# Kernel optimization log

Hardware: AMD Instinct MI355X
Metric: run time of the kernel (lower is better)

Reference implementation:

```python
import jax, jax.numpy as jnp
import numpy as np

B, T, H, S, NH = 8, 4096, 1024, 64, 16
DH = H // NH
L = T // S  # tokens per sentence (contiguous partition)


def setup_inputs() -> dict:
    key = jax.random.key(0)
    ks = jax.random.split(key, 10)
    init = lambda k, shape: (jax.random.normal(k, shape, dtype=jnp.float32) * 0.02)
    starts = jnp.arange(S, dtype=jnp.int32) * L
    bounds = jnp.stack([starts, starts + L], axis=-1)  # [S,2]
    sentence_boundaries = jnp.broadcast_to(bounds, (B, S, 2))
    return {
        "context_hidden": jax.random.normal(ks[0], (B, T, H), dtype=jnp.float32),
        "sentence_boundaries": sentence_boundaries,
        "in_proj_w": init(ks[1], (3 * H, H)),
        "in_proj_b": jnp.zeros((3 * H,), jnp.float32),
        "out_w": init(ks[2], (H, H)),
        "out_b": jnp.zeros((H,), jnp.float32),
        "w1": init(ks[3], (H, 2 * H)),
        "b1": jnp.zeros((H,), jnp.float32),
        "w2": init(ks[4], (1, H)),
        "b2": jnp.zeros((1,), jnp.float32),
    }


def _forward(h, sentence_boundaries, in_proj_w, in_proj_b, out_w, out_b, w1, b1, w2, b2):
    starts = sentence_boundaries[:, :, 0]  # [B,S]
    ends = sentence_boundaries[:, :, 1]    # [B,S]
    t = jnp.arange(T, dtype=jnp.int32)
    # membership: token t belongs to sentence s iff start <= t < end
    member = (t[None, :, None] >= starts[:, None, :]) & (t[None, :, None] < ends[:, None, :])  # [B,T,S]
    mf = member.astype(h.dtype)
    counts = jnp.clip(mf.sum(axis=1), 1.0)  # [B,S]
    # segment mean pooling (encode_sentences)
    sent_repr = jnp.einsum('bts,bth->bsh', mf, h) / counts[..., None]  # [B,S,H]

    # multihead self-attention over sentence reprs (eval mode, no dropout)
    qkv = sent_repr @ in_proj_w.T + in_proj_b  # [B,S,3H]
    q, k, v = jnp.split(qkv, 3, axis=-1)
    q = q.reshape(B, S, NH, DH)
    k = k.reshape(B, S, NH, DH)
    v = v.reshape(B, S, NH, DH)
    scores = jnp.einsum('bqhd,bkhd->bhqk', q, k) / jnp.sqrt(jnp.asarray(DH, h.dtype))
    attn = jax.nn.softmax(scores, axis=-1)
    ctx = jnp.einsum('bhqk,bkhd->bqhd', attn, v).reshape(B, S, H)
    attended = ctx @ out_w.T + out_b  # [B,S,H]

    # gather each token's sentence repr
    sid = jnp.clip(member.astype(jnp.int32).argmax(axis=-1), 0, S - 1)  # [B,T]
    covered = member.any(axis=-1)  # [B,T]
    att_tok = jnp.take_along_axis(attended, sid[..., None], axis=1)  # [B,T,H]

    # coherence scorer MLP on concat([token, sent_repr]) without materializing concat
    hid = jax.nn.relu(h @ w1[:, :H].T + att_tok @ w1[:, H:].T + b1)  # [B,T,H]
    score = (hid @ w2.T + b2)[..., 0]  # [B,T]
    score = jnp.where(covered, score, 0.0)
    return h + score[..., None] * h


def reference(context_hidden, sentence_boundaries, in_proj_w, in_proj_b, out_w, out_b, w1, b1, w2, b2):
    return _forward(context_hidden, sentence_boundaries, in_proj_w, in_proj_b,
                    out_w, out_b, w1, b1, w2, b2)
```

## Files before the change

kernel.cpp:

```cpp
#include <hip/hip_runtime.h>
#include <stdint.h>

#define BB 8
#define TT 4096
#define HH 1024
#define SS 64
#define NHH 16
#define DHH 64

typedef __attribute__((ext_vector_type(8))) short short8;
typedef __attribute__((ext_vector_type(8))) unsigned short ushortx8;
typedef __attribute__((ext_vector_type(4))) float f32x4;
typedef unsigned short u16;

#define GLOAD16(gp, lp)                                                   \
  __builtin_amdgcn_global_load_lds(                                      \
      (const __attribute__((address_space(1))) void*)(gp),               \
      (__attribute__((address_space(3))) void*)(lp), 16, 0, 0)

__device__ __forceinline__ u16 f2bf(float f) {
  union { float f; uint32_t u; } v;
  v.f = f;
  uint32_t u = v.u;
  uint32_t r = u + 0x7fffu + ((u >> 16) & 1u);
  return (u16)(r >> 16);
}

__device__ __forceinline__ float bf2f(u16 b) {
  union { uint32_t u; float f; } v;
  v.u = ((uint32_t)b) << 16;
  return v.f;
}

__device__ __forceinline__ void stage_tile(u16* lds, const float* src, int ld, int tid) {
#pragma unroll
  for (int q = 0; q < 4; ++q) {
    int slot_id = tid + (q << 8);
    int row = slot_id >> 3;
    int sl = slot_id & 7;
    const float* p = src + (size_t)row * ld + (sl << 3);
    float4 x0 = *(const float4*)(p);
    float4 x1 = *(const float4*)(p + 4);
    ushortx8 o;
    o[0] = f2bf(x0.x); o[1] = f2bf(x0.y); o[2] = f2bf(x0.z); o[3] = f2bf(x0.w);
    o[4] = f2bf(x1.x); o[5] = f2bf(x1.y); o[6] = f2bf(x1.z); o[7] = f2bf(x1.w);
    *(ushortx8*)(&lds[(row << 6) + (((sl ^ (row & 7)) << 3))]) = o;
  }
}

__global__ __launch_bounds__(256) void conv_setup_kernel(const float* __restrict__ h,
                                                         u16* __restrict__ hbf,
                                                         const float* __restrict__ w1,
                                                         u16* __restrict__ wbf,
                                                         const float* __restrict__ ipb,
                                                         const float* __restrict__ outb,
                                                         const float* __restrict__ b1,
                                                         const int* __restrict__ bounds,
                                                         float* __restrict__ qkv,
                                                         float* __restrict__ att,
                                                         float* __restrict__ cbuf,
                                                         int* __restrict__ sid) {
  int bid = blockIdx.x;
  int tid = threadIdx.x;
  if (bid >= 4224) {
    int sidx = (bid - 4224) * 256 + tid;
    const int STR = 512 * 256;
    for (int i = sidx; i < 512 * 3072; i += STR) qkv[i] = ipb[i % 3072];
    for (int i = sidx; i < 512 * 1024; i += STR) att[i] = outb[i & 1023];
    for (int i = sidx; i < 512 * 1024; i += STR) cbuf[i] = b1[i & 1023];
    if (sidx < BB * TT) {
      int b = sidx >> 12, t = sidx & (TT - 1);
      int r = -1;
      for (int s = 0; s < SS; ++s) {
        int st = bounds[(b * SS + s) * 2], en = bounds[(b * SS + s) * 2 + 1];
        if (t >= st && t < en) { r = s; break; }
      }
      sid[sidx] = r;
    }
    return;
  }
  const float* src;
  int ld, tbid;
  u16* dst;
  if (bid < 4096) { src = h;  ld = 1024; dst = hbf; tbid = bid; }
  else            { src = w1; ld = 2048; dst = wbf; tbid = bid - 4096; }
  int rt = tbid >> 4, kt = tbid & 15;
  const float* s0 = src + (size_t)rt * 128 * ld + kt * 64;
  u16* d0 = dst + (size_t)tbid * 8192;
#pragma unroll
  for (int q = 0; q < 4; ++q) {
    int slot_id = tid + (q << 8);
    int row = slot_id >> 3;
    int sl = slot_id & 7;
    const float* p = s0 + (size_t)row * ld + (sl << 3);
    float4 x0 = *(const float4*)(p);
    float4 x1 = *(const float4*)(p + 4);
    ushortx8 o;
    o[0] = f2bf(x0.x); o[1] = f2bf(x0.y); o[2] = f2bf(x0.z); o[3] = f2bf(x0.w);
    o[4] = f2bf(x1.x); o[5] = f2bf(x1.y); o[6] = f2bf(x1.z); o[7] = f2bf(x1.w);
    *(ushortx8*)(&d0[(row << 6) + (((sl ^ (row & 7)) << 3))]) = o;
  }
}

__global__ __launch_bounds__(256) void pool_bf_kernel(const u16* __restrict__ hbf,
                                                      const int* __restrict__ bounds,
                                                      float* __restrict__ sent) {
  int bs = blockIdx.x;
  int b = bs >> 6;
  int start = bounds[bs * 2];
  int end = bounds[bs * 2 + 1];
  int lo = max(start, 0), hi = min(end, TT);
  int cnt = max(hi - lo, 0);
  float inv = 1.0f / (float)max(cnt, 1);
  int tid = threadIdx.x;
  int sg = tid >> 1;
  int half = tid & 1;
  int kt = sg >> 3, slot = sg & 7;
  float a[8] = {};
  for (int t = lo + half; t < hi; t += 2) {
    int grow = b * TT + t;
    int rt = grow >> 7, r = grow & 127;
    const u16* tile = hbf + ((size_t)rt * 16 + kt) * 8192;
    ushortx8 v = *(const ushortx8*)(&tile[(r << 6) + ((slot ^ (r & 7)) << 3)]);
#pragma unroll
    for (int j = 0; j < 8; ++j) a[j] += bf2f(v[j]);
  }
#pragma unroll
  for (int j = 0; j < 8; ++j) a[j] += __shfl_xor(a[j], 1);
  if (half == 0) {
    float* d = sent + (size_t)bs * HH + sg * 8;
#pragma unroll
    for (int j = 0; j < 8; ++j) d[j] = a[j] * inv;
  }
}

__global__ __launch_bounds__(256) void gemm_bt_atomic(const float* __restrict__ A, int lda,
                                                      const float* __restrict__ Bm, int ldb,
                                                      float* __restrict__ C, int ldc,
                                                      int kper) {
  __shared__ u16 As[128 * 64];
  __shared__ u16 Bs[128 * 64];
  int tid = threadIdx.x;
  int m0 = blockIdx.x * 128, n0 = blockIdx.y * 128;
  int kbeg = blockIdx.z * kper;
  f32x4 acc[4][4] = {};

  for (int k0 = kbeg; k0 < kbeg + kper; k0 += 64) {
    __syncthreads();
    stage_tile(As, A + (size_t)m0 * lda + k0, lda, tid);
    stage_tile(Bs, Bm + (size_t)n0 * ldb + k0, ldb, tid);
    __syncthreads();
    int lane = tid & 63, wid = tid >> 6;
    int wm = wid >> 1, wn = wid & 1;
    int lr = lane & 15, lg = lane >> 4;
#pragma unroll
    for (int kk = 0; kk < 2; ++kk) {
      short8 af[4], bfr[4];
#pragma unroll
      for (int i = 0; i < 4; ++i) {
        int arow = wm * 64 + i * 16 + lr;
        int aslot = (kk * 4 + lg) ^ (arow & 7);
        af[i] = *(const short8*)(&As[(arow << 6) + (aslot << 3)]);
        int brow = wn * 64 + i * 16 + lr;
        int bslot = (kk * 4 + lg) ^ (brow & 7);
        bfr[i] = *(const short8*)(&Bs[(brow << 6) + (bslot << 3)]);
      }
#pragma unroll
      for (int i = 0; i < 4; ++i)
#pragma unroll
        for (int j = 0; j < 4; ++j)
          acc[i][j] = __builtin_amdgcn_mfma_f32_16x16x32_bf16(af[i], bfr[j], acc[i][j], 0, 0, 0);
    }
  }

  int lane = tid & 63, wid = tid >> 6;
  int wm = wid >> 1, wn = wid & 1;
  int lr = lane & 15, lg = lane >> 4;
#pragma unroll
  for (int i = 0; i < 4; ++i)
#pragma unroll
    for (int j = 0; j < 4; ++j)
#pragma unroll
      for (int r = 0; r < 4; ++r) {
        int row = m0 + wm * 64 + i * 16 + lg * 4 + r;
        int col = n0 + wn * 64 + j * 16 + lr;
        atomicAdd(&C[(size_t)row * ldc + col], acc[i][j][r]);
      }
}

__global__ __launch_bounds__(256) void attn_kernel(const float* __restrict__ qkv,
                                                   float* __restrict__ ctx) {
  int bh = blockIdx.x;
  int b = bh >> 4, nh = bh & 15;
  __shared__ float q[64][64], k[64][64], v[64][64], s[64][64];
  int tid = threadIdx.x;
  const float* base = qkv + (size_t)b * SS * 3072 + nh * 64;
  for (int e = tid; e < 4096; e += 256) {
    int i = e >> 6, d = e & 63;
    q[i][d] = base[(size_t)i * 3072 + d];
    k[i][d] = base[(size_t)i * 3072 + 1024 + d];
    v[i][d] = base[(size_t)i * 3072 + 2048 + d];
  }
  __syncthreads();
  for (int e = tid; e < 4096; e += 256) {
    int i = e >> 6, j = e & 63;
    float acc = 0.f;
#pragma unroll 8
    for (int d = 0; d < 64; ++d) acc += q[i][d] * k[j][d];
    s[i][j] = acc * 0.125f;
  }
  __syncthreads();
  {
    int r = tid >> 2, sub = tid & 3;
    int j0 = sub * 16;
    float m = -1e30f;
#pragma unroll
    for (int j = 0; j < 16; ++j) m = fmaxf(m, s[r][j0 + j]);
    m = fmaxf(m, __shfl_xor(m, 1));
    m = fmaxf(m, __shfl_xor(m, 2));
    float sum = 0.f;
#pragma unroll
    for (int j = 0; j < 16; ++j) {
      float e_ = __expf(s[r][j0 + j] - m);
      s[r][j0 + j] = e_;
      sum += e_;
    }
    sum += __shfl_xor(sum, 1);
    sum += __shfl_xor(sum, 2);
    float inv = 1.0f / sum;
#pragma unroll
    for (int j = 0; j < 16; ++j) s[r][j0 + j] *= inv;
  }
  __syncthreads();
  for (int e = tid; e < 4096; e += 256) {
    int i = e >> 6, d = e & 63;
    float acc = 0.f;
#pragma unroll 8
    for (int j = 0; j < 64; ++j) acc += s[i][j] * v[j][d];
    ctx[((size_t)b * SS + i) * HH + nh * 64 + d] = acc;
  }
}

__global__ __launch_bounds__(512, 4) void score_partial(const u16* __restrict__ hbf,
                                                        const u16* __restrict__ wbf,
                                                        const float* __restrict__ cbuf,
                                                        const float* __restrict__ w2,
                                                        const int* __restrict__ sid_arr,
                                                        float* __restrict__ score_part) {
  __shared__ u16 As[8192];
  __shared__ u16 Bs[16384];
  __shared__ float w2_lds[256];
  __shared__ int sid_lds[128];
  __shared__ float red[128];

  int tid = threadIdx.x;
  int bid = blockIdx.x;
  int x = bid & 7;
  int g = bid >> 3;
  int mt = x * 32 + (g >> 2);
  int c = g & 3;
  int n0 = c * 256;
  size_t g0 = (size_t)mt * 128;
  int b = (int)(g0 >> 12);
  const u16* asrc = hbf + (size_t)mt * 16 * 8192;

  if (tid < 256) w2_lds[tid] = w2[n0 + tid];
  if (tid < 128) {
    sid_lds[tid] = sid_arr[g0 + tid];
    red[tid] = 0.f;
  }

  int lane = tid & 63, wid = tid >> 6;
  int wm = wid >> 2, wn = wid & 3;
  int lr = lane & 15, lg = lane >> 4;

  f32x4 acc[4][4] = {};
  for (int kt = 0; kt < 16; ++kt) {
    __syncthreads();
    const u16* at = asrc + kt * 8192;
#pragma unroll
    for (int q = 0; q < 2; ++q) {
      int off = q * 4096 + wid * 512;
      GLOAD16(at + off + lane * 8, &As[off]);
    }
#pragma unroll
    for (int q = 0; q < 4; ++q) {
      int half = q >> 1;
      int boff = (q & 1) * 4096 + wid * 512;
      const u16* bt = wbf + ((size_t)(2 * c + half) * 16 + kt) * 8192;
      GLOAD16(bt + boff + lane * 8, &Bs[half * 8192 + boff]);
    }
    __syncthreads();
#pragma unroll
    for (int kk = 0; kk < 2; ++kk) {
      short8 af[4], bfr[4];
#pragma unroll
      for (int i = 0; i < 4; ++i) {
        int arow = wm * 64 + i * 16 + lr;
        int aslot = (kk * 4 + lg) ^ (arow & 7);
        af[i] = *(const short8*)(&As[(arow << 6) + (aslot << 3)]);
      }
#pragma unroll
      for (int j = 0; j < 4; ++j) {
        int brow = wn * 64 + j * 16 + lr;
        int half = (wn * 64 + j * 16) >> 7;
        int r = brow & 127;
        int bslot = (kk * 4 + lg) ^ (r & 7);
        bfr[j] = *(const short8*)(&Bs[(half << 13) + (r << 6) + (bslot << 3)]);
      }
#pragma unroll
      for (int i = 0; i < 4; ++i)
#pragma unroll
        for (int j = 0; j < 4; ++j)
          acc[i][j] = __builtin_amdgcn_mfma_f32_16x16x32_bf16(af[i], bfr[j], acc[i][j], 0, 0, 0);
    }
  }

  float sp[4][4];
#pragma unroll
  for (int i = 0; i < 4; ++i) {
#pragma unroll
    for (int r = 0; r < 4; ++r) {
      int rowl = wm * 64 + i * 16 + lg * 4 + r;
      int s = sid_lds[rowl];
      int sc = s < 0 ? 0 : s;
      const float* crow = cbuf + ((size_t)b * SS + sc) * HH + n0;
      float accs = 0.f;
#pragma unroll
      for (int j = 0; j < 4; ++j) {
        int coll = wn * 64 + j * 16 + lr;
        float t = acc[i][j][r] + crow[coll];
        if (t > 0.f) accs += t * w2_lds[coll];
      }
      sp[i][r] = accs;
    }
  }

#pragma unroll
  for (int i = 0; i < 4; ++i)
#pragma unroll
    for (int r = 0; r < 4; ++r) {
      float v = sp[i][r];
      v += __shfl_xor(v, 1);
      v += __shfl_xor(v, 2);
      v += __shfl_xor(v, 4);
      v += __shfl_xor(v, 8);
      sp[i][r] = v;
    }
  if (lr == 0) {
#pragma unroll
    for (int i = 0; i < 4; ++i)
#pragma unroll
      for (int r = 0; r < 4; ++r)
        atomicAdd(&red[wm * 64 + i * 16 + lg * 4 + r], sp[i][r]);
  }
  __syncthreads();
  if (tid < 128) score_part[(size_t)c * (BB * TT) + g0 + tid] = red[tid];
}

__global__ __launch_bounds__(256) void scale_kernel(const u16* __restrict__ hbf,
                                                    const float* __restrict__ score_part,
                                                    const float* __restrict__ b2,
                                                    const int* __restrict__ sid_arr,
                                                    float* __restrict__ out) {
  __shared__ float fac[16];
  int tid = threadIdx.x;
  int r0 = blockIdx.x * 16;
  if (tid < 16) {
    int t = r0 + tid;
    float s = b2[0];
#pragma unroll
    for (int c = 0; c < 4; ++c) s += score_part[(size_t)c * (BB * TT) + t];
    fac[tid] = (sid_arr[t] >= 0) ? (1.0f + s) : 1.0f;
  }
  __syncthreads();
  for (int e = tid; e < 16 * 128; e += 256) {
    int row = e >> 7, grp = e & 127;
    int kt = grp >> 3, slot = grp & 7;
    int grow = r0 + row;
    int rt = grow >> 7, r = grow & 127;
    const u16* tile = hbf + ((size_t)rt * 16 + kt) * 8192;
    ushortx8 v = *(const ushortx8*)(&tile[(r << 6) + ((slot ^ (r & 7)) << 3)]);
    float f = fac[row];
    float4 o0, o1;
    o0.x = bf2f(v[0]) * f; o0.y = bf2f(v[1]) * f; o0.z = bf2f(v[2]) * f; o0.w = bf2f(v[3]) * f;
    o1.x = bf2f(v[4]) * f; o1.y = bf2f(v[5]) * f; o1.z = bf2f(v[6]) * f; o1.w = bf2f(v[7]) * f;
    float4* dst = (float4*)(out + (size_t)grow * HH + grp * 8);
    dst[0] = o0;
    dst[1] = o1;
  }
}

extern "C" void kernel_launch(void* const* d_in, const int* in_sizes, int n_in,
                              void* d_out, int out_size, void* d_ws, size_t ws_size,
                              hipStream_t stream) {
  const float* h        = (const float*)d_in[0];
  const int*   bounds   = (const int*)d_in[1];
  const float* in_proj_w = (const float*)d_in[2];
  const float* in_proj_b = (const float*)d_in[3];
  const float* out_w    = (const float*)d_in[4];
  const float* out_b    = (const float*)d_in[5];
  const float* w1       = (const float*)d_in[6];
  const float* b1       = (const float*)d_in[7];
  const float* w2       = (const float*)d_in[8];
  const float* b2       = (const float*)d_in[9];
  float* out = (float*)d_out;

  char* ws = (char*)d_ws;
  float* sent  = (float*)(ws);
  float* qkv   = (float*)(ws + (2ull << 20));
  float* ctx   = (float*)(ws + (8ull << 20));
  float* att   = (float*)(ws + (10ull << 20));
  float* cbuf  = (float*)(ws + (12ull << 20));
  int*   sid   = (int*)(ws + (14ull << 20));
  float* spart = (float*)(ws + (15ull << 20));
  u16*   hbf   = (u16*)(ws + (16ull << 20));
  u16*   wbf   = (u16*)(ws + (80ull << 20));

  conv_setup_kernel<<<4096 + 128 + 512, 256, 0, stream>>>(
      h, hbf, w1, wbf, in_proj_b, out_b, b1, bounds, qkv, att, cbuf, sid);

  pool_bf_kernel<<<BB * SS, 256, 0, stream>>>(hbf, bounds, sent);

  gemm_bt_atomic<<<dim3(4, 24, 4), 256, 0, stream>>>(sent, HH, in_proj_w, HH, qkv, 3 * HH, 256);
  attn_kernel<<<BB * NHH, 256, 0, stream>>>(qkv, ctx);
  gemm_bt_atomic<<<dim3(4, 8, 4), 256, 0, stream>>>(ctx, HH, out_w, HH, att, HH, 256);
  gemm_bt_atomic<<<dim3(4, 8, 4), 256, 0, stream>>>(att, HH, w1 + HH, 2 * HH, cbuf, HH, 256);

  score_partial<<<1024, 512, 0, stream>>>(hbf, wbf, cbuf, w2, sid, spart);
  scale_kernel<<<2048, 256, 0, stream>>>(hbf, spart, b2, sid, out);
}
```

Measured before the change: 282.5 us.

## Fuse sentence pooling, attention and projection GEMMs into one cooperative kernel

Replaces five small back-to-back launches (pooling, QKV GEMM, attention, out-proj GEMM, w1 GEMM) with a single cooperative kernel of 512 blocks that uses grid-wide syncs between phases. The aim is to remove per-launch overhead and inter-kernel gaps on a chain of tiny kernels. In exchange it adds grid.sync costs, requires all 512 blocks co-resident (the 64KB LDS allocation limits occupancy), and leaves many blocks idle in the later phases.

```diff
diff --git a/kernel.cpp b/kernel.cpp
--- a/kernel.cpp
+++ b/kernel.cpp
@@ -1,5 +1,8 @@
 #include <hip/hip_runtime.h>
+#include <hip/hip_cooperative_groups.h>
 #include <stdint.h>
+
+namespace cg = cooperative_groups;
 
 #define BB 8
 #define TT 4096
@@ -46,6 +49,51 @@
     o[4] = f2bf(x1.x); o[5] = f2bf(x1.y); o[6] = f2bf(x1.z); o[7] = f2bf(x1.w);
     *(ushortx8*)(&lds[(row << 6) + (((sl ^ (row & 7)) << 3))]) = o;
   }
+}
+
+__device__ __forceinline__ void gemm_tile_body(const float* A, int lda,
+                                               const float* Bm, int ldb,
+                                               float* C, int ldc,
+                                               int m0, int n0, int kbeg, int kend,
+                                               u16* As, u16* Bs, int tid) {
+  f32x4 acc[4][4] = {};
+  int lane = tid & 63, wid = tid >> 6;
+  int wm = wid >> 1, wn = wid & 1;
+  int lr = lane & 15, lg = lane >> 4;
+  for (int k0 = kbeg; k0 < kend; k0 += 64) {
+    __syncthreads();
+    stage_tile(As, A + (size_t)m0 * lda + k0, lda, tid);
+    stage_tile(Bs, Bm + (size_t)n0 * ldb + k0, ldb, tid);
+    __syncthreads();
+#pragma unroll
+    for (int kk = 0; kk < 2; ++kk) {
+      short8 af[4], bfr[4];
+#pragma unroll
+      for (int i = 0; i < 4; ++i) {
+        int arow = wm * 64 + i * 16 + lr;
+        int aslot = (kk * 4 + lg) ^ (arow & 7);
+        af[i] = *(const short8*)(&As[(arow << 6) + (aslot << 3)]);
+        int brow = wn * 64 + i * 16 + lr;
+        int bslot = (kk * 4 + lg) ^ (brow & 7);
+        bfr[i] = *(const short8*)(&Bs[(brow << 6) + (bslot << 3)]);
+      }
+#pragma unroll
+      for (int i = 0; i < 4; ++i)
+#pragma unroll
+        for (int j = 0; j < 4; ++j)
+          acc[i][j] = __builtin_amdgcn_mfma_f32_16x16x32_bf16(af[i], bfr[j], acc[i][j], 0, 0, 0);
+    }
+  }
+#pragma unroll
+  for (int i = 0; i < 4; ++i)
+#pragma unroll
+    for (int j = 0; j < 4; ++j)
+#pragma unroll
+      for (int r = 0; r < 4; ++r) {
+        int row = m0 + wm * 64 + i * 16 + lg * 4 + r;
+        int col = n0 + wn * 64 + j * 16 + lr;
+        atomicAdd(&C[(size_t)row * ldc + col], acc[i][j][r]);
+      }
 }
 
 __global__ __launch_bounds__(256) void conv_setup_kernel(const float* __restrict__ h,
@@ -102,142 +150,130 @@
   }
 }
 
-__global__ __launch_bounds__(256) void pool_bf_kernel(const u16* __restrict__ hbf,
+__global__ __launch_bounds__(256) void sentence_chain(const u16* __restrict__ hbf,
                                                       const int* __restrict__ bounds,
-                                                      float* __restrict__ sent) {
-  int bs = blockIdx.x;
-  int b = bs >> 6;
-  int start = bounds[bs * 2];
-  int end = bounds[bs * 2 + 1];
-  int lo = max(start, 0), hi = min(end, TT);
-  int cnt = max(hi - lo, 0);
-  float inv = 1.0f / (float)max(cnt, 1);
+                                                      const float* __restrict__ ipw,
+                                                      const float* __restrict__ outw,
+                                                      const float* __restrict__ w1,
+                                                      float* __restrict__ sent,
+                                                      float* __restrict__ qkv,
+                                                      float* __restrict__ ctx,
+                                                      float* __restrict__ att,
+                                                      float* __restrict__ cbuf) {
+  cg::grid_group grid = cg::this_grid();
+  __shared__ __align__(16) char lds_raw[65536];
+  u16* As = (u16*)lds_raw;
+  u16* Bs = (u16*)(lds_raw + 16384);
+  float* ldsf = (float*)lds_raw;
+
+  int bid = blockIdx.x;
   int tid = threadIdx.x;
-  int sg = tid >> 1;
-  int half = tid & 1;
-  int kt = sg >> 3, slot = sg & 7;
-  float a[8] = {};
-  for (int t = lo + half; t < hi; t += 2) {
-    int grow = b * TT + t;
-    int rt = grow >> 7, r = grow & 127;
-    const u16* tile = hbf + ((size_t)rt * 16 + kt) * 8192;
-    ushortx8 v = *(const ushortx8*)(&tile[(r << 6) + ((slot ^ (r & 7)) << 3)]);
-#pragma unroll
-    for (int j = 0; j < 8; ++j) a[j] += bf2f(v[j]);
-  }
-#pragma unroll
-  for (int j = 0; j < 8; ++j) a[j] += __shfl_xor(a[j], 1);
-  if (half == 0) {
-    float* d = sent + (size_t)bs * HH + sg * 8;
-#pragma unroll
-    for (int j = 0; j < 8; ++j) d[j] = a[j] * inv;
-  }
-}
-
-__global__ __launch_bounds__(256) void gemm_bt_atomic(const float* __restrict__ A, int lda,
-                                                      const float* __restrict__ Bm, int ldb,
-                                                      float* __restrict__ C, int ldc,
-                                                      int kper) {
-  __shared__ u16 As[128 * 64];
-  __shared__ u16 Bs[128 * 64];
-  int tid = threadIdx.x;
-  int m0 = blockIdx.x * 128, n0 = blockIdx.y * 128;
-  int kbeg = blockIdx.z * kper;
-  f32x4 acc[4][4] = {};
-
-  for (int k0 = kbeg; k0 < kbeg + kper; k0 += 64) {
-    __syncthreads();
-    stage_tile(As, A + (size_t)m0 * lda + k0, lda, tid);
-    stage_tile(Bs, Bm + (size_t)n0 * ldb + k0, ldb, tid);
-    __syncthreads();
-    int lane = tid & 63, wid = tid >> 6;
-    int wm = wid >> 1, wn = wid & 1;
-    int lr = lane & 15, lg = lane >> 4;
-#pragma unroll
-    for (int kk = 0; kk < 2; ++kk) {
-      short8 af[4], bfr[4];
-#pragma unroll
-      for (int i = 0; i < 4; ++i) {
-        int arow = wm * 64 + i * 16 + lr;
-        int aslot = (kk * 4 + lg) ^ (arow & 7);
-        af[i] = *(const short8*)(&As[(arow << 6) + (aslot << 3)]);
-        int brow = wn * 64 + i * 16 + lr;
-        int bslot = (kk * 4 + lg) ^ (brow & 7);
-        bfr[i] = *(const short8*)(&Bs[(brow << 6) + (bslot << 3)]);
-      }
-#pragma unroll
-      for (int i = 0; i < 4; ++i)
-#pragma unroll
-        for (int j = 0; j < 4; ++j)
-          acc[i][j] = __builtin_amdgcn_mfma_f32_16x16x32_bf16(af[i], bfr[j], acc[i][j], 0, 0, 0);
-    }
-  }
-
-  int lane = tid & 63, wid = tid >> 6;
-  int wm = wid >> 1, wn = wid & 1;
-  int lr = lane & 15, lg = lane >> 4;
-#pragma unroll
-  for (int i = 0; i < 4; ++i)
-#pragma unroll
-    for (int j = 0; j < 4; ++j)
-#pragma unroll
-      for (int r = 0; r < 4; ++r) {
-        int row = m0 + wm * 64 + i * 16 + lg * 4 + r;
-        int col = n0 + wn * 64 + j * 16 + lr;
-        atomicAdd(&C[(size_t)row * ldc + col], acc[i][j][r]);
-      }
-}
-
-__global__ __launch_bounds__(256) void attn_kernel(const float* __restrict__ qkv,
-                                                   float* __restrict__ ctx) {
-  int bh = blockIdx.x;
-  int b = bh >> 4, nh = bh & 15;
-  __shared__ float q[64][64], k[64][64], v[64][64], s[64][64];
-  int tid = threadIdx.x;
-  const float* base = qkv + (size_t)b * SS * 3072 + nh * 64;
-  for (int e = tid; e < 4096; e += 256) {
-    int i = e >> 6, d = e & 63;
-    q[i][d] = base[(size_t)i * 3072 + d];
-    k[i][d] = base[(size_t)i * 3072 + 1024 + d];
-    v[i][d] = base[(size_t)i * 3072 + 2048 + d];
-  }
-  __syncthreads();
-  for (int e = tid; e < 4096; e += 256) {
-    int i = e >> 6, j = e & 63;
-    float acc = 0.f;
+
+  {
+    int bs = bid;
+    int b = bs >> 6;
+    int start = bounds[bs * 2];
+    int end = bounds[bs * 2 + 1];
+    int lo = max(start, 0), hi = min(end, TT);
+    int cnt = max(hi - lo, 0);
+    float inv = 1.0f / (float)max(cnt, 1);
+    int sg = tid >> 1;
+    int half = tid & 1;
+    int kt = sg >> 3, slot = sg & 7;
+    float a[8] = {};
+    for (int t = lo + half; t < hi; t += 2) {
+      int grow = b * TT + t;
+      int rt = grow >> 7, r = grow & 127;
+      const u16* tile = hbf + ((size_t)rt * 16 + kt) * 8192;
+      ushortx8 v = *(const ushortx8*)(&tile[(r << 6) + ((slot ^ (r & 7)) << 3)]);
+#pragma unroll
+      for (int j = 0; j < 8; ++j) a[j] += bf2f(v[j]);
+    }
+#pragma unroll
+    for (int j = 0; j < 8; ++j) a[j] += __shfl_xor(a[j], 1);
+    if (half == 0) {
+      float* d = sent + (size_t)bs * HH + sg * 8;
+#pragma unroll
+      for (int j = 0; j < 8; ++j) d[j] = a[j] * inv;
+    }
+  }
+  grid.sync();
+
+  if (bid < 384) {
+    int t = bid % 96, kz = bid / 96;
+    int mt = t & 3, nt = t >> 2;
+    gemm_tile_body(sent, HH, ipw, HH, qkv, 3 * HH,
+                   mt * 128, nt * 128, kz * 256, kz * 256 + 256, As, Bs, tid);
+  }
+  grid.sync();
+
+  if (bid < 128) {
+    int b = bid >> 4, nh = bid & 15;
+    float* q = ldsf;
+    float* k = ldsf + 4096;
+    float* v = ldsf + 8192;
+    float* s = ldsf + 12288;
+    const float* base = qkv + (size_t)b * SS * 3072 + nh * 64;
+    for (int e = tid; e < 4096; e += 256) {
+      int i = e >> 6, d = e & 63;
+      q[e] = base[(size_t)i * 3072 + d];
+      k[e] = base[(size_t)i * 3072 + 1024 + d];
+      v[e] = base[(size_t)i * 3072 + 2048 + d];
+    }
+    __syncthreads();
+    for (int e = tid; e < 4096; e += 256) {
+      int i = e >> 6, j = e & 63;
+      float acc = 0.f;
 #pragma unroll 8
-    for (int d = 0; d < 64; ++d) acc += q[i][d] * k[j][d];
-    s[i][j] = acc * 0.125f;
-  }
-  __syncthreads();
-  {
-    int r = tid >> 2, sub = tid & 3;
-    int j0 = sub * 16;
-    float m = -1e30f;
-#pragma unroll
-    for (int j = 0; j < 16; ++j) m = fmaxf(m, s[r][j0 + j]);
-    m = fmaxf(m, __shfl_xor(m, 1));
-    m = fmaxf(m, __shfl_xor(m, 2));
-    float sum = 0.f;
-#pragma unroll
-    for (int j = 0; j < 16; ++j) {
-      float e_ = __expf(s[r][j0 + j] - m);
-      s[r][j0 + j] = e_;
-      sum += e_;
-    }
-    sum += __shfl_xor(sum, 1);
-    sum += __shfl_xor(sum, 2);
-    float inv = 1.0f / sum;
-#pragma unroll
-    for (int j = 0; j < 16; ++j) s[r][j0 + j] *= inv;
-  }
-  __syncthreads();
-  for (int e = tid; e < 4096; e += 256) {
-    int i = e >> 6, d = e & 63;
-    float acc = 0.f;
+      for (int d = 0; d < 64; ++d) acc += q[i * 64 + d] * k[j * 64 + d];
+      s[e] = acc * 0.125f;
+    }
+    __syncthreads();
+    {
+      int r = tid >> 2, sub = tid & 3;
+      int j0 = sub * 16;
+      float m = -1e30f;
+#pragma unroll
+      for (int j = 0; j < 16; ++j) m = fmaxf(m, s[r * 64 + j0 + j]);
+      m = fmaxf(m, __shfl_xor(m, 1));
+      m = fmaxf(m, __shfl_xor(m, 2));
+      float sum = 0.f;
+#pragma unroll
+      for (int j = 0; j < 16; ++j) {
+        float e_ = __expf(s[r * 64 + j0 + j] - m);
+        s[r * 64 + j0 + j] = e_;
+        sum += e_;
+      }
+      sum += __shfl_xor(sum, 1);
+      sum += __shfl_xor(sum, 2);
+      float inv = 1.0f / sum;
+#pragma unroll
+      for (int j = 0; j < 16; ++j) s[r * 64 + j0 + j] *= inv;
+    }
+    __syncthreads();
+    for (int e = tid; e < 4096; e += 256) {
+      int i = e >> 6, d = e & 63;
+      float acc = 0.f;
 #pragma unroll 8
-    for (int j = 0; j < 64; ++j) acc += s[i][j] * v[j][d];
-    ctx[((size_t)b * SS + i) * HH + nh * 64 + d] = acc;
+      for (int j = 0; j < 64; ++j) acc += s[i * 64 + j] * v[j * 64 + d];
+      ctx[((size_t)b * SS + i) * HH + nh * 64 + d] = acc;
+    }
+  }
+  grid.sync();
+
+  if (bid < 128) {
+    int t = bid % 32, kz = bid / 32;
+    int mt = t & 3, nt = t >> 2;
+    gemm_tile_body(ctx, HH, outw, HH, att, HH,
+                   mt * 128, nt * 128, kz * 256, kz * 256 + 256, As, Bs, tid);
+  }
+  grid.sync();
+
+  if (bid < 128) {
+    int t = bid % 32, kz = bid / 32;
+    int mt = t & 3, nt = t >> 2;
+    gemm_tile_body(att, HH, w1 + HH, 2 * HH, cbuf, HH,
+                   mt * 128, nt * 128, kz * 256, kz * 256 + 256, As, Bs, tid);
   }
 }
 
@@ -420,12 +456,23 @@
   conv_setup_kernel<<<4096 + 128 + 512, 256, 0, stream>>>(
       h, hbf, w1, wbf, in_proj_b, out_b, b1, bounds, qkv, att, cbuf, sid);
 
-  pool_bf_kernel<<<BB * SS, 256, 0, stream>>>(hbf, bounds, sent);
-
-  gemm_bt_atomic<<<dim3(4, 24, 4), 256, 0, stream>>>(sent, HH, in_proj_w, HH, qkv, 3 * HH, 256);
-  attn_kernel<<<BB * NHH, 256, 0, stream>>>(qkv, ctx);
-  gemm_bt_atomic<<<dim3(4, 8, 4), 256, 0, stream>>>(ctx, HH, out_w, HH, att, HH, 256);
-  gemm_bt_atomic<<<dim3(4, 8, 4), 256, 0, stream>>>(att, HH, w1 + HH, 2 * HH, cbuf, HH, 256);
+  {
+    const u16* hbf_a = hbf;
+    const int* bounds_a = bounds;
+    const float* ipw_a = in_proj_w;
+    const float* outw_a = out_w;
+    const float* w1_a = w1;
+    float* sent_a = sent;
+    float* qkv_a = qkv;
+    float* ctx_a = ctx;
+    float* att_a = att;
+    float* cbuf_a = cbuf;
+    void* args[] = {(void*)&hbf_a, (void*)&bounds_a, (void*)&ipw_a, (void*)&outw_a,
+                    (void*)&w1_a, (void*)&sent_a, (void*)&qkv_a, (void*)&ctx_a,
+                    (void*)&att_a, (void*)&cbuf_a};
+    hipLaunchCooperativeKernel((const void*)sentence_chain, dim3(512), dim3(256),
+                               args, 0, stream);
+  }
 
   score_partial<<<1024, 512, 0, stream>>>(hbf, wbf, cbuf, w2, sid, spart);
   scale_kernel<<<2048, 256, 0, stream>>>(hbf, spart, b2, sid, out);
```

New measurement: 514.3 us. 1.82x slower.

## Fuse sentence pooling into setup kernel from fp32 input; swizzle attention LDS

Applied to the files above, without the earlier changes.

Removes the separate pooling launch. Mean pooling now runs as 512 extra blocks in the setup kernel, reading the fp32 hidden states directly rather than the bf16 tiled copy, which lets pooling run alongside the conversion and also changes pooling precision from bf16 to fp32. The attention kernel's K and score shared-memory arrays get an XOR column swizzle to cut bank conflicts on the strided row accesses. In exchange, pooling re-reads fp32 h, twice the bytes of the bf16 copy, competing for bandwidth with the conversion blocks.

```diff
diff --git a/kernel.cpp b/kernel.cpp
--- a/kernel.cpp
+++ b/kernel.cpp
@@ -59,9 +59,43 @@
                                                          float* __restrict__ qkv,
                                                          float* __restrict__ att,
                                                          float* __restrict__ cbuf,
-                                                         int* __restrict__ sid) {
+                                                         int* __restrict__ sid,
+                                                         float* __restrict__ sent) {
   int bid = blockIdx.x;
   int tid = threadIdx.x;
+  if (bid >= 4736) {
+    int bs = bid - 4736;
+    int b = bs >> 6;
+    int start = bounds[bs * 2];
+    int end = bounds[bs * 2 + 1];
+    int lo = max(start, 0), hi = min(end, TT);
+    int cnt = max(hi - lo, 0);
+    float inv = 1.0f / (float)max(cnt, 1);
+    const float4* h4 = (const float4*)(h) + (size_t)b * TT * 256 + tid;
+    float4 a0 = {0, 0, 0, 0}, a1 = {0, 0, 0, 0}, a2 = {0, 0, 0, 0}, a3 = {0, 0, 0, 0};
+    int t = lo;
+    for (; t + 4 <= hi; t += 4) {
+      float4 v0 = h4[(size_t)(t + 0) * 256];
+      float4 v1 = h4[(size_t)(t + 1) * 256];
+      float4 v2 = h4[(size_t)(t + 2) * 256];
+      float4 v3 = h4[(size_t)(t + 3) * 256];
+      a0.x += v0.x; a0.y += v0.y; a0.z += v0.z; a0.w += v0.w;
+      a1.x += v1.x; a1.y += v1.y; a1.z += v1.z; a1.w += v1.w;
+      a2.x += v2.x; a2.y += v2.y; a2.z += v2.z; a2.w += v2.w;
+      a3.x += v3.x; a3.y += v3.y; a3.z += v3.z; a3.w += v3.w;
+    }
+    for (; t < hi; ++t) {
+      float4 v0 = h4[(size_t)t * 256];
+      a0.x += v0.x; a0.y += v0.y; a0.z += v0.z; a0.w += v0.w;
+    }
+    float4 r;
+    r.x = (a0.x + a1.x + a2.x + a3.x) * inv;
+    r.y = (a0.y + a1.y + a2.y + a3.y) * inv;
+    r.z = (a0.z + a1.z + a2.z + a3.z) * inv;
+    r.w = (a0.w + a1.w + a2.w + a3.w) * inv;
+    ((float4*)sent)[(size_t)bs * 256 + tid] = r;
+    return;
+  }
   if (bid >= 4224) {
     int sidx = (bid - 4224) * 256 + tid;
     const int STR = 512 * 256;
@@ -102,38 +136,6 @@
   }
 }
 
-__global__ __launch_bounds__(256) void pool_bf_kernel(const u16* __restrict__ hbf,
-                                                      const int* __restrict__ bounds,
-                                                      float* __restrict__ sent) {
-  int bs = blockIdx.x;
-  int b = bs >> 6;
-  int start = bounds[bs * 2];
-  int end = bounds[bs * 2 + 1];
-  int lo = max(start, 0), hi = min(end, TT);
-  int cnt = max(hi - lo, 0);
-  float inv = 1.0f / (float)max(cnt, 1);
-  int tid = threadIdx.x;
-  int sg = tid >> 1;
-  int half = tid & 1;
-  int kt = sg >> 3, slot = sg & 7;
-  float a[8] = {};
-  for (int t = lo + half; t < hi; t += 2) {
-    int grow = b * TT + t;
-    int rt = grow >> 7, r = grow & 127;
-    const u16* tile = hbf + ((size_t)rt * 16 + kt) * 8192;
-    ushortx8 v = *(const ushortx8*)(&tile[(r << 6) + ((slot ^ (r & 7)) << 3)]);
-#pragma unroll
-    for (int j = 0; j < 8; ++j) a[j] += bf2f(v[j]);
-  }
-#pragma unroll
-  for (int j = 0; j < 8; ++j) a[j] += __shfl_xor(a[j], 1);
-  if (half == 0) {
-    float* d = sent + (size_t)bs * HH + sg * 8;
-#pragma unroll
-    for (int j = 0; j < 8; ++j) d[j] = a[j] * inv;
-  }
-}
-
 __global__ __launch_bounds__(256) void gemm_bt_atomic(const float* __restrict__ A, int lda,
                                                       const float* __restrict__ Bm, int ldb,
                                                       float* __restrict__ C, int ldc,
@@ -188,26 +190,27 @@
       }
 }
 
+#define KSW(row, col) (((row) << 6) + ((col) ^ (row)))
 __global__ __launch_bounds__(256) void attn_kernel(const float* __restrict__ qkv,
                                                    float* __restrict__ ctx) {
   int bh = blockIdx.x;
   int b = bh >> 4, nh = bh & 15;
-  __shared__ float q[64][64], k[64][64], v[64][64], s[64][64];
+  __shared__ float q[64 * 64], k[64 * 64], v[64 * 64], s[64 * 64];
   int tid = threadIdx.x;
   const float* base = qkv + (size_t)b * SS * 3072 + nh * 64;
   for (int e = tid; e < 4096; e += 256) {
     int i = e >> 6, d = e & 63;
-    q[i][d] = base[(size_t)i * 3072 + d];
-    k[i][d] = base[(size_t)i * 3072 + 1024 + d];
-    v[i][d] = base[(size_t)i * 3072 + 2048 + d];
+    q[e] = base[(size_t)i * 3072 + d];
+    k[KSW(i, d)] = base[(size_t)i * 3072 + 1024 + d];
+    v[e] = base[(size_t)i * 3072 + 2048 + d];
   }
   __syncthreads();
   for (int e = tid; e < 4096; e += 256) {
     int i = e >> 6, j = e & 63;
     float acc = 0.f;
 #pragma unroll 8
-    for (int d = 0; d < 64; ++d) acc += q[i][d] * k[j][d];
-    s[i][j] = acc * 0.125f;
+    for (int d = 0; d < 64; ++d) acc += q[(i << 6) + d] * k[KSW(j, d)];
+    s[KSW(i, j)] = acc * 0.125f;
   }
   __syncthreads();
   {
@@ -215,28 +218,28 @@
     int j0 = sub * 16;
     float m = -1e30f;
 #pragma unroll
-    for (int j = 0; j < 16; ++j) m = fmaxf(m, s[r][j0 + j]);
+    for (int j = 0; j < 16; ++j) m = fmaxf(m, s[KSW(r, j0 + j)]);
     m = fmaxf(m, __shfl_xor(m, 1));
     m = fmaxf(m, __shfl_xor(m, 2));
     float sum = 0.f;
 #pragma unroll
     for (int j = 0; j < 16; ++j) {
-      float e_ = __expf(s[r][j0 + j] - m);
-      s[r][j0 + j] = e_;
+      float e_ = __expf(s[KSW(r, j0 + j)] - m);
+      s[KSW(r, j0 + j)] = e_;
       sum += e_;
     }
     sum += __shfl_xor(sum, 1);
     sum += __shfl_xor(sum, 2);
     float inv = 1.0f / sum;
 #pragma unroll
-    for (int j = 0; j < 16; ++j) s[r][j0 + j] *= inv;
+    for (int j = 0; j < 16; ++j) s[KSW(r, j0 + j)] *= inv;
   }
   __syncthreads();
   for (int e = tid; e < 4096; e += 256) {
     int i = e >> 6, d = e & 63;
     float acc = 0.f;
 #pragma unroll 8
-    for (int j = 0; j < 64; ++j) acc += s[i][j] * v[j][d];
+    for (int j = 0; j < 64; ++j) acc += s[KSW(i, j)] * v[(j << 6) + d];
     ctx[((size_t)b * SS + i) * HH + nh * 64 + d] = acc;
   }
 }
@@ -417,10 +420,8 @@
   u16*   hbf   = (u16*)(ws + (16ull << 20));
   u16*   wbf   = (u16*)(ws + (80ull << 20));
 
-  conv_setup_kernel<<<4096 + 128 + 512, 256, 0, stream>>>(
-      h, hbf, w1, wbf, in_proj_b, out_b, b1, bounds, qkv, att, cbuf, sid);
-
-  pool_bf_kernel<<<BB * SS, 256, 0, stream>>>(hbf, bounds, sent);
+  conv_setup_kernel<<<4096 + 128 + 512 + 512, 256, 0, stream>>>(
+      h, hbf, w1, wbf, in_proj_b, out_b, b1, bounds, qkv, att, cbuf, sid, sent);
 
   gemm_bt_atomic<<<dim3(4, 24, 4), 256, 0, stream>>>(sent, HH, in_proj_w, HH, qkv, 3 * HH, 256);
   attn_kernel<<<BB * NHH, 256, 0, stream>>>(qkv, ctx);
```

Result: faster. 275.9 us (-2.3%).
